# Kernel optimization log

Measured on AMD Instinct MI355X. Metric: run time of the kernel, lower is better.

## Reference

```python
import jax, jax.numpy as jnp
import numpy as np

B, NCAMS = 1, 6
C_FEAT = 64                     # fusion_feat_in_dim
H, W = 88, 160                  # per-camera feature map size at fusion level
VOX_SIZE = (100, 100, 20)       # (x_dim, y_dim, z_dim) voxel counts
VOX_STR = (-50.0, -50.0, -15.0)
VOX_UNIT = (1.0, 1.0, 1.5)
N_VOX = VOX_SIZE[0] * VOX_SIZE[1] * VOX_SIZE[2]
EPS = 1e-8
V_PRE = 64                      # voxel_pre_dim[0]


def make_voxel_pts(dtype):
    # [B, 4, N]; homogeneous (x, y, z, 1) points, layout [z, y, x] flattened
    xs = jnp.linspace(VOX_STR[0], VOX_STR[0] + VOX_UNIT[0] * (VOX_SIZE[0] - 1), VOX_SIZE[0], dtype=dtype)
    ys = jnp.linspace(VOX_STR[1], VOX_STR[1] + VOX_UNIT[1] * (VOX_SIZE[1] - 1), VOX_SIZE[1], dtype=dtype)
    zs = jnp.linspace(VOX_STR[2], VOX_STR[2] + VOX_UNIT[2] * (VOX_SIZE[2] - 1), VOX_SIZE[2], dtype=dtype)
    zdim, ydim, xdim = VOX_SIZE[2], VOX_SIZE[1], VOX_SIZE[0]
    gx = jnp.broadcast_to(xs[None, None, :], (zdim, ydim, xdim)).reshape(-1)
    gy = jnp.broadcast_to(ys[None, :, None], (zdim, ydim, xdim)).reshape(-1)
    gz = jnp.broadcast_to(zs[:, None, None], (zdim, ydim, xdim)).reshape(-1)
    pts = jnp.stack([gx, gy, gz, jnp.ones_like(gx)], axis=0)  # [4, N]
    return jnp.broadcast_to(pts[None], (B, 4, N_VOX))


def _gather(imgf, iy, ix, Wd):
    # imgf: [BN, C, H*W]; iy/ix: [BN, N] int32 -> [BN, C, N]
    lin = iy * Wd + ix
    return jnp.take_along_axis(imgf, lin[:, None, :], axis=2)


def bilinear_sample(img, gx, gy):
    # grid_sample(mode='bilinear', padding_mode='zeros', align_corners=True)
    BN, C, Hd, Wd = img.shape
    x = (gx + 1.0) * 0.5 * (Wd - 1)
    y = (gy + 1.0) * 0.5 * (Hd - 1)
    x0 = jnp.floor(x); y0 = jnp.floor(y)
    wx1 = x - x0; wx0 = 1.0 - wx1
    wy1 = y - y0; wy0 = 1.0 - wy1
    imgf = img.reshape(BN, C, Hd * Wd)
    out = jnp.zeros((BN, C, gx.shape[1]), dtype=img.dtype)
    for xi, wxi in ((x0, wx0), (x0 + 1.0, wx1)):
        for yi, wyi in ((y0, wy0), (y0 + 1.0, wy1)):
            valid = (xi >= 0) & (xi <= Wd - 1) & (yi >= 0) & (yi <= Hd - 1)
            ii = jnp.clip(xi, 0, Wd - 1).astype(jnp.int32)
            jj = jnp.clip(yi, 0, Hd - 1).astype(jnp.int32)
            w = (wxi * wyi * valid.astype(img.dtype))[:, None, :]
            out = out + _gather(imgf, jj, ii, Wd) * w
    return out


def nearest_sample(img, gx, gy):
    # grid_sample(mode='nearest', padding_mode='zeros', align_corners=True)
    BN, C, Hd, Wd = img.shape
    x = (gx + 1.0) * 0.5 * (Wd - 1)
    y = (gy + 1.0) * 0.5 * (Hd - 1)
    xi = jnp.round(x); yi = jnp.round(y)
    valid = (xi >= 0) & (xi <= Wd - 1) & (yi >= 0) & (yi <= Hd - 1)
    ii = jnp.clip(xi, 0, Wd - 1).astype(jnp.int32)
    jj = jnp.clip(yi, 0, Hd - 1).astype(jnp.int32)
    imgf = img.reshape(BN, C, Hd * Wd)
    return _gather(imgf, jj, ii, Wd) * valid[:, None, :].astype(img.dtype)


def setup_inputs() -> dict:
    key = jax.random.key(0)
    ks = jax.random.split(key, 8)
    return {
        'multi_img_feat': jax.random.normal(ks[0], (B, NCAMS, C_FEAT, H, W), jnp.float32),
        'mask': jax.random.uniform(ks[1], (B, NCAMS, 1, H, W), jnp.float32),
        'K': jax.random.normal(ks[2], (B, NCAMS, 4, 4), jnp.float32),
        'extrinsics': jax.random.normal(ks[3], (B, NCAMS, 4, 4), jnp.float32),
        'w_no': jax.random.normal(ks[4], (V_PRE, C_FEAT + 1), jnp.float32) * 0.05,
        'b_no': jax.random.normal(ks[5], (V_PRE,), jnp.float32) * 0.05,
        'w_o': jax.random.normal(ks[6], (V_PRE, 2 * (C_FEAT + 1)), jnp.float32) * 0.05,
        'b_o': jax.random.normal(ks[7], (V_PRE,), jnp.float32) * 0.05,
    }


def reference(multi_img_feat, mask, K, extrinsics, w_no, b_no, w_o, b_o):
    Bb, NC, C, Hd, Wd = multi_img_feat.shape
    dt = multi_img_feat.dtype
    vpts = make_voxel_pts(dt)                                          # [B,4,N]
    vpts_c = jnp.broadcast_to(vpts[:, None], (Bb, NC, 4, N_VOX)).reshape(Bb * NC, 4, N_VOX)
    feats = multi_img_feat.reshape(Bb * NC, C, Hd, Wd)
    masks = mask.reshape(Bb * NC, 1, Hd, Wd)                           # interp to (H,W) is identity (same size, align_corners)
    ext = extrinsics.reshape(Bb * NC, 4, 4)[:, :3, :]
    K3 = K.reshape(Bb * NC, 4, 4)[:, :3, :3]

    v_local = jnp.einsum('bij,bjn->bin', ext, vpts_c)                  # [BN,3,N]
    cam_pts = jnp.einsum('bij,bjn->bin', K3, v_local)
    pix = cam_pts[:, :2] / (cam_pts[:, 2:3] + EPS)
    pix = jnp.where(jnp.all(jnp.isfinite(pix)), pix, jnp.clip(pix, -Wd * 2.0, Wd * 2.0))
    gx = (pix[:, 0] / (Wd - 1) - 0.5) * 2.0                            # [BN,N] normalized coords
    gy = (pix[:, 1] / (Hd - 1) - 0.5) * 2.0

    feat_w = bilinear_sample(feats, gx, gy)                            # [BN,C,N]
    m_occ = nearest_sample(masks, gx, gy) > 0.5                        # [BN,1,N]
    m_depth = v_local[:, 2:3] > 0
    oob = (gx > 1) | (gx < -1) | (gy > 1) | (gy < -1)
    valid = (m_occ & m_depth & (~oob)[:, None, :]).astype(dt)          # [BN,1,N]

    feat_w = jnp.concatenate([feat_w, v_local[:, 2:3] / VOX_SIZE[0]], axis=1) * valid  # [BN,C+1,N]

    feat_w = feat_w.reshape(Bb, NC, C + 1, N_VOX)
    valid = valid.reshape(Bb, NC, 1, N_VOX)
    count = valid.sum(axis=1)                                          # [B,1,N]

    # non-overlap branch: voxels seen by exactly one camera
    no_mask = (count == 1).astype(dt)
    vox_no = feat_w.sum(axis=1) * no_mask
    vox_no = jax.nn.elu(jnp.einsum('oc,bcn->bon', w_no, vox_no) + b_no[None, :, None]) * no_mask

    # overlap branch: cams {0,3,4} vs {1,2,5}
    o_mask = (count == 2).astype(dt)
    feat1 = feat_w[:, 0] + feat_w[:, 3] + feat_w[:, 4]
    feat2 = feat_w[:, 1] + feat_w[:, 2] + feat_w[:, 5]
    vox_o = jnp.concatenate([feat1, feat2], axis=1)                    # [B,2*(C+1),N]
    vox_o = jax.nn.elu(jnp.einsum('oc,bcn->bon', w_o, vox_o) + b_o[None, :, None]) * o_mask

    return vox_no + vox_o                                              # [B, V_PRE, N]
```

## Files before the change

### kernel.cpp

```cpp
#include <hip/hip_runtime.h>
#include <cmath>

#define NC 6
#define CF 64
#define HH 88
#define WW 160
#define NPIX 14080
#define NVOX 200000
#define VPRE 64
#define VB 128
#define NTH 512
#define NWV 8

typedef unsigned int u32;

#define FEATT_BYTES  (6u * 64u * 14080u * 4u)

__global__ __launch_bounds__(256) void transpose_feats(const float* __restrict__ in,
                                                       float* __restrict__ out) {
    __shared__ float tile[64 * 65];
    int blk = blockIdx.x;
    int c = blk / 220;
    int p0 = (blk - c * 220) * 64;
    int tid = threadIdx.x;
    int lane = tid & 63;
    int quad = tid >> 6;
    for (int r = quad; r < 64; r += 4)
        tile[r * 65 + lane] = in[(c * 64 + r) * NPIX + p0 + lane];
    __syncthreads();
    for (int r = quad; r < 64; r += 4)
        out[((c * NPIX) + p0 + r) * 64 + lane] = tile[lane * 65 + r];
}

__device__ __forceinline__ float elu1(float x) { return x > 0.0f ? x : expm1f(x); }

__device__ __forceinline__ float gather_bilin(const float* __restrict__ fsrc, int useT,
                                              int lane, int cam, float x, float y) {
    float x0f = floorf(x), y0f = floorf(y);
    float wx1 = x - x0f, wx0 = 1.0f - wx1;
    float wy1 = y - y0f, wy0 = 1.0f - wy1;
    float x1f = x0f + 1.0f, y1f = y0f + 1.0f;
    float bx0 = (x0f >= 0.0f && x0f <= 159.0f) ? 1.0f : 0.0f;
    float bx1 = (x1f >= 0.0f && x1f <= 159.0f) ? 1.0f : 0.0f;
    float by0 = (y0f >= 0.0f && y0f <= 87.0f) ? 1.0f : 0.0f;
    float by1 = (y1f >= 0.0f && y1f <= 87.0f) ? 1.0f : 0.0f;
    int ix0 = (int)fminf(fmaxf(x0f, 0.0f), 159.0f);
    int ix1 = (int)fminf(fmaxf(x1f, 0.0f), 159.0f);
    int iy0 = (int)fminf(fmaxf(y0f, 0.0f), 87.0f);
    int iy1 = (int)fminf(fmaxf(y1f, 0.0f), 87.0f);
    int A = useT ? 64 : 1;
    int Boff = useT ? (cam * NPIX * 64 + lane) : ((cam * 64 + lane) * NPIX);
    float v00 = fsrc[(iy0 * WW + ix0) * A + Boff];
    float v01 = fsrc[(iy1 * WW + ix0) * A + Boff];
    float v10 = fsrc[(iy0 * WW + ix1) * A + Boff];
    float v11 = fsrc[(iy1 * WW + ix1) * A + Boff];
    float fv;
    fv  = (wx0 * wy0 * bx0 * by0) * v00;
    fv += (wx0 * wy1 * bx0 * by1) * v01;
    fv += (wx1 * wy0 * bx1 * by0) * v10;
    fv += (wx1 * wy1 * bx1 * by1) * v11;
    return fv;
}

#define FMA8_STEP(W0,W1,W2,W3,W4,W5,W6,W7,CG,F0,F1,F2,F3) \
    a0 += W0[CG]*F0; a0 += W0[CG+1]*F1; a0 += W0[CG+2]*F2; a0 += W0[CG+3]*F3; \
    a1 += W1[CG]*F0; a1 += W1[CG+1]*F1; a1 += W1[CG+2]*F2; a1 += W1[CG+3]*F3; \
    a2 += W2[CG]*F0; a2 += W2[CG+1]*F1; a2 += W2[CG+2]*F2; a2 += W2[CG+3]*F3; \
    a3 += W3[CG]*F0; a3 += W3[CG+1]*F1; a3 += W3[CG+2]*F2; a3 += W3[CG+3]*F3; \
    a4 += W4[CG]*F0; a4 += W4[CG+1]*F1; a4 += W4[CG+2]*F2; a4 += W4[CG+3]*F3; \
    a5 += W5[CG]*F0; a5 += W5[CG+1]*F1; a5 += W5[CG+2]*F2; a5 += W5[CG+3]*F3; \
    a6 += W6[CG]*F0; a6 += W6[CG+1]*F1; a6 += W6[CG+2]*F2; a6 += W6[CG+3]*F3; \
    a7 += W7[CG]*F0; a7 += W7[CG+1]*F1; a7 += W7[CG+2]*F2; a7 += W7[CG+3]*F3;

#define STORE8(COL) \
    outp[(size_t)(obase + 0) * NVOX + COL] = elu1(a0); \
    outp[(size_t)(obase + 1) * NVOX + COL] = elu1(a1); \
    outp[(size_t)(obase + 2) * NVOX + COL] = elu1(a2); \
    outp[(size_t)(obase + 3) * NVOX + COL] = elu1(a3); \
    outp[(size_t)(obase + 4) * NVOX + COL] = elu1(a4); \
    outp[(size_t)(obase + 5) * NVOX + COL] = elu1(a5); \
    outp[(size_t)(obase + 6) * NVOX + COL] = elu1(a6); \
    outp[(size_t)(obase + 7) * NVOX + COL] = elu1(a7);

__global__ __launch_bounds__(NTH) void vox_fused(
    const float* __restrict__ feats,
    const float* __restrict__ featT,
    const float* __restrict__ mask,
    const float* __restrict__ Kg,
    const float* __restrict__ ext,
    const float* __restrict__ wno,
    const float* __restrict__ bno,
    const float* __restrict__ wo,
    const float* __restrict__ bo,
    float* __restrict__ outp,
    int useT)
{
    __shared__ float s_ext[72];
    __shared__ float s_K[54];
    __shared__ float s_F[65 * 66];
    __shared__ __align__(16) float4 s_rec1[VB];
    __shared__ __align__(16) float4 s_rec2[2 * VB];
    __shared__ int s_vox[64];
    __shared__ int s_n1, s_n2;

    int tid = threadIdx.x;
    int lane = tid & 63;
    int wv = tid >> 6;
    int base = blockIdx.x * VB;
    int vlim = min(VB, NVOX - base);

    if (tid == 0) { s_n1 = 0; s_n2 = 0; }
    if (tid >= 64 && tid < 136) {
        int i = tid - 64;
        s_ext[i] = ext[(i / 12) * 16 + (i % 12)];
    }
    if (tid >= 192 && tid < 246) {
        int i = tid - 192; int cam = i / 9; int e = i - cam * 9;
        s_K[i] = Kg[cam * 16 + (e / 3) * 4 + (e % 3)];
    }

    {
        int ng4 = vlim >> 2;
        for (int i = tid; i < 64 * (VB / 4); i += NTH) {
            int r = i >> 5, cg = i & ((VB / 4) - 1);
            if (cg < ng4)
                *(float4*)(outp + (size_t)r * NVOX + base + (cg << 2)) =
                    make_float4(0.f, 0.f, 0.f, 0.f);
        }
    }
    __syncthreads();

    if (tid < vlim) {
        #pragma clang fp contract(off)
        int n = base + tid;
        int xi = n % 100;
        int t = n / 100;
        int yi = t % 100;
        int zi = t / 100;
        float X = -50.0f + (float)xi;
        float Y = -50.0f + (float)yi;
        float Z = -15.0f + 1.5f * (float)zi;
        int cnt = 0, cam0 = 0, cam1 = 0;
        float ax = 0.f, ay = 0.f, az = 0.f, bx = 0.f, by = 0.f, bz = 0.f;
        #pragma unroll
        for (int cam = 0; cam < NC; ++cam) {
            const float* E = s_ext + cam * 12;
            const float* Kk = s_K + cam * 9;
            float vl0 = E[0]*X + E[1]*Y + E[2]*Z + E[3];
            float vl1 = E[4]*X + E[5]*Y + E[6]*Z + E[7];
            float vl2 = E[8]*X + E[9]*Y + E[10]*Z + E[11];
            float c0 = Kk[0]*vl0 + Kk[1]*vl1 + Kk[2]*vl2;
            float c1 = Kk[3]*vl0 + Kk[4]*vl1 + Kk[5]*vl2;
            float c2 = Kk[6]*vl0 + Kk[7]*vl1 + Kk[8]*vl2;
            float pz = c2 + 1e-8f;
            float px = c0 / pz;
            float py = c1 / pz;
            float gx = (px / 159.0f - 0.5f) * 2.0f;
            float gy = (py / 87.0f - 0.5f) * 2.0f;
            float x = ((gx + 1.0f) * 0.5f) * 159.0f;
            float y = ((gy + 1.0f) * 0.5f) * 87.0f;
            float xr = rintf(x), yr = rintf(y);
            bool nv = (xr >= 0.0f) && (xr <= 159.0f) && (yr >= 0.0f) && (yr <= 87.0f);
            float mval = 0.0f;
            if (nv) mval = mask[(cam * HH + (int)yr) * WW + (int)xr];
            bool ok = (mval > 0.5f) && (vl2 > 0.0f) &&
                      !((gx > 1.0f) || (gx < -1.0f) || (gy > 1.0f) || (gy < -1.0f));
            if (ok) {
                if (cnt == 0) { ax = x; ay = y; az = vl2; cam0 = cam; }
                else if (cnt == 1) { bx = x; by = y; bz = vl2; cam1 = cam; }
                ++cnt;
            }
        }
        if (cnt == 1) {
            int s = atomicAdd(&s_n1, 1);
            s_rec1[s] = make_float4(ax, ay, az, __int_as_float((n << 3) | cam0));
        } else if (cnt == 2) {
            int s = atomicAdd(&s_n2, 1);
            s_rec2[2 * s + 0] = make_float4(ax, ay, az, __int_as_float((n << 3) | cam0));
            s_rec2[2 * s + 1] = make_float4(bx, by, bz, __int_as_float((n << 3) | cam1));
        }
    }
    __syncthreads();

    int n1 = s_n1, n2 = s_n2;
    const float* fsrc = useT ? featT : feats;
    int wvu = __builtin_amdgcn_readfirstlane(wv);
    int obase = wvu * 8;
    const float* w0n = wno + (obase + 0) * 65;
    const float* w1n = wno + (obase + 1) * 65;
    const float* w2n = wno + (obase + 2) * 65;
    const float* w3n = wno + (obase + 3) * 65;
    const float* w4n = wno + (obase + 4) * 65;
    const float* w5n = wno + (obase + 5) * 65;
    const float* w6n = wno + (obase + 6) * 65;
    const float* w7n = wno + (obase + 7) * 65;
    const float* w0o = wo + (obase + 0) * 130;
    const float* w1o = wo + (obase + 1) * 130;
    const float* w2o = wo + (obase + 2) * 130;
    const float* w3o = wo + (obase + 3) * 130;
    const float* w4o = wo + (obase + 4) * 130;
    const float* w5o = wo + (obase + 5) * 130;
    const float* w6o = wo + (obase + 6) * 130;
    const float* w7o = wo + (obase + 7) * 130;

    for (int t0 = 0; t0 < n1; t0 += 64) {
        int tl = min(64, n1 - t0);
        for (int e = wv; e < tl; e += NWV) {
            float4 r = s_rec1[t0 + e];
            int meta = __float_as_int(r.w);
            int cam = meta & 7;
            float fv = gather_bilin(fsrc, useT, lane, cam, r.x, r.y);
            s_F[lane * 66 + e] = fv;
            if (lane == 0) { s_F[64 * 66 + e] = r.z / 100.0f; s_vox[e] = meta >> 3; }
        }
        __syncthreads();
        float a0 = bno[obase + 0], a1 = bno[obase + 1], a2 = bno[obase + 2], a3 = bno[obase + 3];
        float a4 = bno[obase + 4], a5 = bno[obase + 5], a6 = bno[obase + 6], a7 = bno[obase + 7];
        for (int cg = 0; cg < 64; cg += 4) {
            float f0 = s_F[(cg + 0) * 66 + lane];
            float f1 = s_F[(cg + 1) * 66 + lane];
            float f2 = s_F[(cg + 2) * 66 + lane];
            float f3 = s_F[(cg + 3) * 66 + lane];
            FMA8_STEP(w0n, w1n, w2n, w3n, w4n, w5n, w6n, w7n, cg, f0, f1, f2, f3)
        }
        float fd = s_F[64 * 66 + lane];
        a0 += w0n[64] * fd; a1 += w1n[64] * fd; a2 += w2n[64] * fd; a3 += w3n[64] * fd;
        a4 += w4n[64] * fd; a5 += w5n[64] * fd; a6 += w6n[64] * fd; a7 += w7n[64] * fd;
        if (lane < tl) {
            size_t col = (size_t)s_vox[lane];
            STORE8(col)
        }
        __syncthreads();
    }

    for (int t0 = 0; t0 < n2; t0 += 64) {
        int tl = min(64, n2 - t0);
        for (int e = wv; e < tl; e += NWV) {
            float4 r0 = s_rec2[2 * (t0 + e) + 0];
            float4 r1 = s_rec2[2 * (t0 + e) + 1];
            int m0 = __float_as_int(r0.w), m1 = __float_as_int(r1.w);
            int ca = m0 & 7, cb = m1 & 7;
            float fg = 0.0f, dd = 0.0f;
            if (!(ca == 1 || ca == 2 || ca == 5)) {
                fg += gather_bilin(fsrc, useT, lane, ca, r0.x, r0.y);
                dd += r0.z / 100.0f;
            }
            if (!(cb == 1 || cb == 2 || cb == 5)) {
                fg += gather_bilin(fsrc, useT, lane, cb, r1.x, r1.y);
                dd += r1.z / 100.0f;
            }
            s_F[lane * 66 + e] = fg;
            if (lane == 0) { s_F[64 * 66 + e] = dd; s_vox[e] = m0 >> 3; }
        }
        __syncthreads();
        float a0 = bo[obase + 0], a1 = bo[obase + 1], a2 = bo[obase + 2], a3 = bo[obase + 3];
        float a4 = bo[obase + 4], a5 = bo[obase + 5], a6 = bo[obase + 6], a7 = bo[obase + 7];
        for (int cg = 0; cg < 64; cg += 4) {
            float f0 = s_F[(cg + 0) * 66 + lane];
            float f1 = s_F[(cg + 1) * 66 + lane];
            float f2 = s_F[(cg + 2) * 66 + lane];
            float f3 = s_F[(cg + 3) * 66 + lane];
            FMA8_STEP(w0o, w1o, w2o, w3o, w4o, w5o, w6o, w7o, cg, f0, f1, f2, f3)
        }
        {
            float fd = s_F[64 * 66 + lane];
            a0 += w0o[64] * fd; a1 += w1o[64] * fd; a2 += w2o[64] * fd; a3 += w3o[64] * fd;
            a4 += w4o[64] * fd; a5 += w5o[64] * fd; a6 += w6o[64] * fd; a7 += w7o[64] * fd;
        }
        __syncthreads();
        for (int e = wv; e < tl; e += NWV) {
            float4 r0 = s_rec2[2 * (t0 + e) + 0];
            float4 r1 = s_rec2[2 * (t0 + e) + 1];
            int m0 = __float_as_int(r0.w), m1 = __float_as_int(r1.w);
            int ca = m0 & 7, cb = m1 & 7;
            float fg = 0.0f, dd = 0.0f;
            if (ca == 1 || ca == 2 || ca == 5) {
                fg += gather_bilin(fsrc, useT, lane, ca, r0.x, r0.y);
                dd += r0.z / 100.0f;
            }
            if (cb == 1 || cb == 2 || cb == 5) {
                fg += gather_bilin(fsrc, useT, lane, cb, r1.x, r1.y);
                dd += r1.z / 100.0f;
            }
            s_F[lane * 66 + e] = fg;
            if (lane == 0) s_F[64 * 66 + e] = dd;
        }
        __syncthreads();
        for (int cg = 0; cg < 64; cg += 4) {
            float f0 = s_F[(cg + 0) * 66 + lane];
            float f1 = s_F[(cg + 1) * 66 + lane];
            float f2 = s_F[(cg + 2) * 66 + lane];
            float f3 = s_F[(cg + 3) * 66 + lane];
            int cgo = cg + 65;
            FMA8_STEP(w0o, w1o, w2o, w3o, w4o, w5o, w6o, w7o, cgo, f0, f1, f2, f3)
        }
        {
            float fd = s_F[64 * 66 + lane];
            a0 += w0o[129] * fd; a1 += w1o[129] * fd; a2 += w2o[129] * fd; a3 += w3o[129] * fd;
            a4 += w4o[129] * fd; a5 += w5o[129] * fd; a6 += w6o[129] * fd; a7 += w7o[129] * fd;
        }
        if (lane < tl) {
            size_t col = (size_t)s_vox[lane];
            STORE8(col)
        }
        __syncthreads();
    }
}

extern "C" void kernel_launch(void* const* d_in, const int* in_sizes, int n_in,
                              void* d_out, int out_size, void* d_ws, size_t ws_size,
                              hipStream_t stream) {
    const float* feats = (const float*)d_in[0];
    const float* mask  = (const float*)d_in[1];
    const float* Kg    = (const float*)d_in[2];
    const float* ext   = (const float*)d_in[3];
    const float* wno   = (const float*)d_in[4];
    const float* bno   = (const float*)d_in[5];
    const float* wo    = (const float*)d_in[6];
    const float* bo    = (const float*)d_in[7];
    float* outp = (float*)d_out;
    float* featT = (float*)d_ws;

    int useT = (ws_size >= (size_t)FEATT_BYTES) ? 1 : 0;
    if (useT) {
        transpose_feats<<<NC * 220, 256, 0, stream>>>(feats, featT);
    }
    int nblk = (NVOX + VB - 1) / VB;
    vox_fused<<<nblk, NTH, 0, stream>>>(feats, featT, mask, Kg, ext,
                                        wno, bno, wo, bo, outp, useT);
}
```

Before: 162.5 us.

## Defer overlap-voxel work to a compacted global queue processed by a second kernel

```diff
diff --git a/kernel.cpp b/kernel.cpp
--- a/kernel.cpp
+++ b/kernel.cpp
@@ -8,16 +8,21 @@
 #define NPIX 14080
 #define NVOX 200000
 #define VPRE 64
-#define VB 128
+#define VB 192
 #define NTH 512
 #define NWV 8
 
 typedef unsigned int u32;
 
 #define FEATT_BYTES  (6u * 64u * 14080u * 4u)
+#define REC2_OFF     FEATT_BYTES
+#define REC2_BYTES   (200000u * 32u)
+#define CNT_OFF      (REC2_OFF + REC2_BYTES)
+#define WS_NEED      (CNT_OFF + 16u)
 
 __global__ __launch_bounds__(256) void transpose_feats(const float* __restrict__ in,
-                                                       float* __restrict__ out) {
+                                                       float* __restrict__ out,
+                                                       int* __restrict__ cnt) {
     __shared__ float tile[64 * 65];
     int blk = blockIdx.x;
     int c = blk / 220;
@@ -25,6 +30,7 @@
     int tid = threadIdx.x;
     int lane = tid & 63;
     int quad = tid >> 6;
+    if (cnt && blk == 0 && tid == 0) cnt[0] = 0;
     for (int r = quad; r < 64; r += 4)
         tile[r * 65 + lane] = in[(c * 64 + r) * NPIX + p0 + lane];
     __syncthreads();
@@ -82,6 +88,26 @@
     outp[(size_t)(obase + 6) * NVOX + COL] = elu1(a6); \
     outp[(size_t)(obase + 7) * NVOX + COL] = elu1(a7);
 
+#define WNO_PTRS \
+    const float* w0n = wno + (obase + 0) * 65; \
+    const float* w1n = wno + (obase + 1) * 65; \
+    const float* w2n = wno + (obase + 2) * 65; \
+    const float* w3n = wno + (obase + 3) * 65; \
+    const float* w4n = wno + (obase + 4) * 65; \
+    const float* w5n = wno + (obase + 5) * 65; \
+    const float* w6n = wno + (obase + 6) * 65; \
+    const float* w7n = wno + (obase + 7) * 65;
+
+#define WO_PTRS \
+    const float* w0o = wo + (obase + 0) * 130; \
+    const float* w1o = wo + (obase + 1) * 130; \
+    const float* w2o = wo + (obase + 2) * 130; \
+    const float* w3o = wo + (obase + 3) * 130; \
+    const float* w4o = wo + (obase + 4) * 130; \
+    const float* w5o = wo + (obase + 5) * 130; \
+    const float* w6o = wo + (obase + 6) * 130; \
+    const float* w7o = wo + (obase + 7) * 130;
+
 __global__ __launch_bounds__(NTH) void vox_fused(
     const float* __restrict__ feats,
     const float* __restrict__ featT,
@@ -93,7 +119,9 @@
     const float* __restrict__ wo,
     const float* __restrict__ bo,
     float* __restrict__ outp,
-    int useT)
+    float4* __restrict__ grec2,
+    int* __restrict__ gcnt,
+    int useT, int defer2)
 {
     __shared__ float s_ext[72];
     __shared__ float s_K[54];
@@ -101,7 +129,7 @@
     __shared__ __align__(16) float4 s_rec1[VB];
     __shared__ __align__(16) float4 s_rec2[2 * VB];
     __shared__ int s_vox[64];
-    __shared__ int s_n1, s_n2;
+    __shared__ int s_n1, s_n2, s_base2;
 
     int tid = threadIdx.x;
     int lane = tid & 63;
@@ -110,19 +138,19 @@
     int vlim = min(VB, NVOX - base);
 
     if (tid == 0) { s_n1 = 0; s_n2 = 0; }
-    if (tid >= 64 && tid < 136) {
-        int i = tid - 64;
+    if (tid >= 256 && tid < 328) {
+        int i = tid - 256;
         s_ext[i] = ext[(i / 12) * 16 + (i % 12)];
     }
-    if (tid >= 192 && tid < 246) {
-        int i = tid - 192; int cam = i / 9; int e = i - cam * 9;
+    if (tid >= 384 && tid < 438) {
+        int i = tid - 384; int cam = i / 9; int e = i - cam * 9;
         s_K[i] = Kg[cam * 16 + (e / 3) * 4 + (e % 3)];
     }
 
     {
         int ng4 = vlim >> 2;
         for (int i = tid; i < 64 * (VB / 4); i += NTH) {
-            int r = i >> 5, cg = i & ((VB / 4) - 1);
+            int r = i / (VB / 4), cg = i - r * (VB / 4);
             if (cg < ng4)
                 *(float4*)(outp + (size_t)r * NVOX + base + (cg << 2)) =
                     make_float4(0.f, 0.f, 0.f, 0.f);
@@ -186,22 +214,17 @@
     const float* fsrc = useT ? featT : feats;
     int wvu = __builtin_amdgcn_readfirstlane(wv);
     int obase = wvu * 8;
-    const float* w0n = wno + (obase + 0) * 65;
-    const float* w1n = wno + (obase + 1) * 65;
-    const float* w2n = wno + (obase + 2) * 65;
-    const float* w3n = wno + (obase + 3) * 65;
-    const float* w4n = wno + (obase + 4) * 65;
-    const float* w5n = wno + (obase + 5) * 65;
-    const float* w6n = wno + (obase + 6) * 65;
-    const float* w7n = wno + (obase + 7) * 65;
-    const float* w0o = wo + (obase + 0) * 130;
-    const float* w1o = wo + (obase + 1) * 130;
-    const float* w2o = wo + (obase + 2) * 130;
-    const float* w3o = wo + (obase + 3) * 130;
-    const float* w4o = wo + (obase + 4) * 130;
-    const float* w5o = wo + (obase + 5) * 130;
-    const float* w6o = wo + (obase + 6) * 130;
-    const float* w7o = wo + (obase + 7) * 130;
+    WNO_PTRS
+
+    if (defer2) {
+        if (n2 > 0) {
+            if (tid == 0) s_base2 = atomicAdd(gcnt, n2);
+            __syncthreads();
+            int b2 = s_base2;
+            for (int i = tid; i < 2 * n2; i += NTH)
+                grec2[2 * b2 + i] = s_rec2[i];
+        }
+    }
 
     for (int t0 = 0; t0 < n1; t0 += 64) {
         int tl = min(64, n1 - t0);
@@ -233,11 +256,113 @@
         __syncthreads();
     }
 
-    for (int t0 = 0; t0 < n2; t0 += 64) {
-        int tl = min(64, n2 - t0);
+    if (!defer2) {
+        WO_PTRS
+        for (int t0 = 0; t0 < n2; t0 += 64) {
+            int tl = min(64, n2 - t0);
+            for (int e = wv; e < tl; e += NWV) {
+                float4 r0 = s_rec2[2 * (t0 + e) + 0];
+                float4 r1 = s_rec2[2 * (t0 + e) + 1];
+                int m0 = __float_as_int(r0.w), m1 = __float_as_int(r1.w);
+                int ca = m0 & 7, cb = m1 & 7;
+                float fg = 0.0f, dd = 0.0f;
+                if (!(ca == 1 || ca == 2 || ca == 5)) {
+                    fg += gather_bilin(fsrc, useT, lane, ca, r0.x, r0.y);
+                    dd += r0.z / 100.0f;
+                }
+                if (!(cb == 1 || cb == 2 || cb == 5)) {
+                    fg += gather_bilin(fsrc, useT, lane, cb, r1.x, r1.y);
+                    dd += r1.z / 100.0f;
+                }
+                s_F[lane * 66 + e] = fg;
+                if (lane == 0) { s_F[64 * 66 + e] = dd; s_vox[e] = m0 >> 3; }
+            }
+            __syncthreads();
+            float a0 = bo[obase + 0], a1 = bo[obase + 1], a2 = bo[obase + 2], a3 = bo[obase + 3];
+            float a4 = bo[obase + 4], a5 = bo[obase + 5], a6 = bo[obase + 6], a7 = bo[obase + 7];
+            for (int cg = 0; cg < 64; cg += 4) {
+                float f0 = s_F[(cg + 0) * 66 + lane];
+                float f1 = s_F[(cg + 1) * 66 + lane];
+                float f2 = s_F[(cg + 2) * 66 + lane];
+                float f3 = s_F[(cg + 3) * 66 + lane];
+                FMA8_STEP(w0o, w1o, w2o, w3o, w4o, w5o, w6o, w7o, cg, f0, f1, f2, f3)
+            }
+            {
+                float fd = s_F[64 * 66 + lane];
+                a0 += w0o[64] * fd; a1 += w1o[64] * fd; a2 += w2o[64] * fd; a3 += w3o[64] * fd;
+                a4 += w4o[64] * fd; a5 += w5o[64] * fd; a6 += w6o[64] * fd; a7 += w7o[64] * fd;
+            }
+            __syncthreads();
+            for (int e = wv; e < tl; e += NWV) {
+                float4 r0 = s_rec2[2 * (t0 + e) + 0];
+                float4 r1 = s_rec2[2 * (t0 + e) + 1];
+                int m0 = __float_as_int(r0.w), m1 = __float_as_int(r1.w);
+                int ca = m0 & 7, cb = m1 & 7;
+                float fg = 0.0f, dd = 0.0f;
+                if (ca == 1 || ca == 2 || ca == 5) {
+                    fg += gather_bilin(fsrc, useT, lane, ca, r0.x, r0.y);
+                    dd += r0.z / 100.0f;
+                }
+                if (cb == 1 || cb == 2 || cb == 5) {
+                    fg += gather_bilin(fsrc, useT, lane, cb, r1.x, r1.y);
+                    dd += r1.z / 100.0f;
+                }
+                s_F[lane * 66 + e] = fg;
+                if (lane == 0) s_F[64 * 66 + e] = dd;
+            }
+            __syncthreads();
+            for (int cg = 0; cg < 64; cg += 4) {
+                float f0 = s_F[(cg + 0) * 66 + lane];
+                float f1 = s_F[(cg + 1) * 66 + lane];
+                float f2 = s_F[(cg + 2) * 66 + lane];
+                float f3 = s_F[(cg + 3) * 66 + lane];
+                int cgo = cg + 65;
+                FMA8_STEP(w0o, w1o, w2o, w3o, w4o, w5o, w6o, w7o, cgo, f0, f1, f2, f3)
+            }
+            {
+                float fd = s_F[64 * 66 + lane];
+                a0 += w0o[129] * fd; a1 += w1o[129] * fd; a2 += w2o[129] * fd; a3 += w3o[129] * fd;
+                a4 += w4o[129] * fd; a5 += w5o[129] * fd; a6 += w6o[129] * fd; a7 += w7o[129] * fd;
+            }
+            if (lane < tl) {
+                size_t col = (size_t)s_vox[lane];
+                STORE8(col)
+            }
+            __syncthreads();
+        }
+    }
+}
+
+__global__ __launch_bounds__(NTH) void vox_ov(
+    const float* __restrict__ feats,
+    const float* __restrict__ featT,
+    const float4* __restrict__ rec2,
+    const int* __restrict__ gcnt,
+    const float* __restrict__ wo,
+    const float* __restrict__ bo,
+    float* __restrict__ outp,
+    int useT)
+{
+    __shared__ float s_F[65 * 66];
+    __shared__ int s_vox[64];
+
+    int tid = threadIdx.x;
+    int lane = tid & 63;
+    int wv = tid >> 6;
+    int c2 = gcnt[0];
+    int nt = (c2 + 63) >> 6;
+
+    const float* fsrc = useT ? featT : feats;
+    int wvu = __builtin_amdgcn_readfirstlane(wv);
+    int obase = wvu * 8;
+    WO_PTRS
+
+    for (int t = blockIdx.x; t < nt; t += gridDim.x) {
+        int e0 = t << 6;
+        int tl = min(64, c2 - e0);
         for (int e = wv; e < tl; e += NWV) {
-            float4 r0 = s_rec2[2 * (t0 + e) + 0];
-            float4 r1 = s_rec2[2 * (t0 + e) + 1];
+            float4 r0 = rec2[2 * (e0 + e) + 0];
+            float4 r1 = rec2[2 * (e0 + e) + 1];
             int m0 = __float_as_int(r0.w), m1 = __float_as_int(r1.w);
             int ca = m0 & 7, cb = m1 & 7;
             float fg = 0.0f, dd = 0.0f;
@@ -269,8 +394,8 @@
         }
         __syncthreads();
         for (int e = wv; e < tl; e += NWV) {
-            float4 r0 = s_rec2[2 * (t0 + e) + 0];
-            float4 r1 = s_rec2[2 * (t0 + e) + 1];
+            float4 r0 = rec2[2 * (e0 + e) + 0];
+            float4 r1 = rec2[2 * (e0 + e) + 1];
             int m0 = __float_as_int(r0.w), m1 = __float_as_int(r1.w);
             int ca = m0 & 7, cb = m1 & 7;
             float fg = 0.0f, dd = 0.0f;
@@ -319,13 +444,23 @@
     const float* wo    = (const float*)d_in[6];
     const float* bo    = (const float*)d_in[7];
     float* outp = (float*)d_out;
-    float* featT = (float*)d_ws;
+    char* wsb = (char*)d_ws;
+    float* featT = (float*)wsb;
 
     int useT = (ws_size >= (size_t)FEATT_BYTES) ? 1 : 0;
+    int defer2 = (ws_size >= (size_t)WS_NEED) ? 1 : 0;
+    float4* grec2 = defer2 ? (float4*)(wsb + REC2_OFF) : nullptr;
+    int* gcnt = defer2 ? (int*)(wsb + CNT_OFF) : nullptr;
+
     if (useT) {
-        transpose_feats<<<NC * 220, 256, 0, stream>>>(feats, featT);
+        transpose_feats<<<NC * 220, 256, 0, stream>>>(feats, featT, gcnt);
     }
     int nblk = (NVOX + VB - 1) / VB;
     vox_fused<<<nblk, NTH, 0, stream>>>(feats, featT, mask, Kg, ext,
-                                        wno, bno, wo, bo, outp, useT);
+                                        wno, bno, wo, bo, outp,
+                                        grec2, gcnt, useT, defer2);
+    if (defer2) {
+        vox_ov<<<256, NTH, 0, stream>>>(feats, featT, grec2, gcnt,
+                                        wo, bo, outp, useT);
+    }
 }
```

Result: slower. 174.4 us (+7.3%).

## Unroll bilinear gather loops, batch LDS feature reads, and enlarge voxel block

Applied to the files above, without the earlier changes.

```diff
diff --git a/kernel.cpp b/kernel.cpp
--- a/kernel.cpp
+++ b/kernel.cpp
@@ -8,7 +8,7 @@
 #define NPIX 14080
 #define NVOX 200000
 #define VPRE 64
-#define VB 128
+#define VB 192
 #define NTH 512
 #define NWV 8
 
@@ -82,6 +82,18 @@
     outp[(size_t)(obase + 6) * NVOX + COL] = elu1(a6); \
     outp[(size_t)(obase + 7) * NVOX + COL] = elu1(a7);
 
+#define COMPUTE_HALF(WB0,WB1,WB2,WB3,WB4,WB5,WB6,WB7,CBASE) \
+    { \
+        float f[32]; \
+        _Pragma("unroll") \
+        for (int c = 0; c < 32; ++c) f[c] = s_F[(CBASE + c) * 66 + lane]; \
+        _Pragma("unroll") \
+        for (int cg = 0; cg < 32; cg += 4) { \
+            FMA8_STEP(WB0,WB1,WB2,WB3,WB4,WB5,WB6,WB7, (CBASE + cg), \
+                      f[cg], f[cg+1], f[cg+2], f[cg+3]) \
+        } \
+    }
+
 __global__ __launch_bounds__(NTH) void vox_fused(
     const float* __restrict__ feats,
     const float* __restrict__ featT,
@@ -110,19 +122,19 @@
     int vlim = min(VB, NVOX - base);
 
     if (tid == 0) { s_n1 = 0; s_n2 = 0; }
-    if (tid >= 64 && tid < 136) {
-        int i = tid - 64;
+    if (tid >= 256 && tid < 328) {
+        int i = tid - 256;
         s_ext[i] = ext[(i / 12) * 16 + (i % 12)];
     }
-    if (tid >= 192 && tid < 246) {
-        int i = tid - 192; int cam = i / 9; int e = i - cam * 9;
+    if (tid >= 384 && tid < 438) {
+        int i = tid - 384; int cam = i / 9; int e = i - cam * 9;
         s_K[i] = Kg[cam * 16 + (e / 3) * 4 + (e % 3)];
     }
 
     {
         int ng4 = vlim >> 2;
         for (int i = tid; i < 64 * (VB / 4); i += NTH) {
-            int r = i >> 5, cg = i & ((VB / 4) - 1);
+            int r = i / (VB / 4), cg = i - r * (VB / 4);
             if (cg < ng4)
                 *(float4*)(outp + (size_t)r * NVOX + base + (cg << 2)) =
                     make_float4(0.f, 0.f, 0.f, 0.f);
@@ -205,24 +217,25 @@
 
     for (int t0 = 0; t0 < n1; t0 += 64) {
         int tl = min(64, n1 - t0);
-        for (int e = wv; e < tl; e += NWV) {
-            float4 r = s_rec1[t0 + e];
+        int tl1 = tl - 1;
+        #pragma unroll
+        for (int j = 0; j < 8; ++j) {
+            int e = wv + j * NWV;
+            int ee = min(e, tl1);
+            float4 r = s_rec1[t0 + ee];
             int meta = __float_as_int(r.w);
             int cam = meta & 7;
             float fv = gather_bilin(fsrc, useT, lane, cam, r.x, r.y);
-            s_F[lane * 66 + e] = fv;
-            if (lane == 0) { s_F[64 * 66 + e] = r.z / 100.0f; s_vox[e] = meta >> 3; }
+            if (e < tl) {
+                s_F[lane * 66 + e] = fv;
+                if (lane == 0) { s_F[64 * 66 + e] = r.z / 100.0f; s_vox[e] = meta >> 3; }
+            }
         }
         __syncthreads();
         float a0 = bno[obase + 0], a1 = bno[obase + 1], a2 = bno[obase + 2], a3 = bno[obase + 3];
         float a4 = bno[obase + 4], a5 = bno[obase + 5], a6 = bno[obase + 6], a7 = bno[obase + 7];
-        for (int cg = 0; cg < 64; cg += 4) {
-            float f0 = s_F[(cg + 0) * 66 + lane];
-            float f1 = s_F[(cg + 1) * 66 + lane];
-            float f2 = s_F[(cg + 2) * 66 + lane];
-            float f3 = s_F[(cg + 3) * 66 + lane];
-            FMA8_STEP(w0n, w1n, w2n, w3n, w4n, w5n, w6n, w7n, cg, f0, f1, f2, f3)
-        }
+        COMPUTE_HALF(w0n, w1n, w2n, w3n, w4n, w5n, w6n, w7n, 0)
+        COMPUTE_HALF(w0n, w1n, w2n, w3n, w4n, w5n, w6n, w7n, 32)
         float fd = s_F[64 * 66 + lane];
         a0 += w0n[64] * fd; a1 += w1n[64] * fd; a2 += w2n[64] * fd; a3 += w3n[64] * fd;
         a4 += w4n[64] * fd; a5 += w5n[64] * fd; a6 += w6n[64] * fd; a7 += w7n[64] * fd;
@@ -235,9 +248,13 @@
 
     for (int t0 = 0; t0 < n2; t0 += 64) {
         int tl = min(64, n2 - t0);
-        for (int e = wv; e < tl; e += NWV) {
-            float4 r0 = s_rec2[2 * (t0 + e) + 0];
-            float4 r1 = s_rec2[2 * (t0 + e) + 1];
+        int tl1 = tl - 1;
+        #pragma unroll
+        for (int j = 0; j < 8; ++j) {
+            int e = wv + j * NWV;
+            int ee = min(e, tl1);
+            float4 r0 = s_rec2[2 * (t0 + ee) + 0];
+            float4 r1 = s_rec2[2 * (t0 + ee) + 1];
             int m0 = __float_as_int(r0.w), m1 = __float_as_int(r1.w);
             int ca = m0 & 7, cb = m1 & 7;
             float fg = 0.0f, dd = 0.0f;
@@ -249,28 +266,28 @@
                 fg += gather_bilin(fsrc, useT, lane, cb, r1.x, r1.y);
                 dd += r1.z / 100.0f;
             }
-            s_F[lane * 66 + e] = fg;
-            if (lane == 0) { s_F[64 * 66 + e] = dd; s_vox[e] = m0 >> 3; }
+            if (e < tl) {
+                s_F[lane * 66 + e] = fg;
+                if (lane == 0) { s_F[64 * 66 + e] = dd; s_vox[e] = m0 >> 3; }
+            }
         }
         __syncthreads();
         float a0 = bo[obase + 0], a1 = bo[obase + 1], a2 = bo[obase + 2], a3 = bo[obase + 3];
         float a4 = bo[obase + 4], a5 = bo[obase + 5], a6 = bo[obase + 6], a7 = bo[obase + 7];
-        for (int cg = 0; cg < 64; cg += 4) {
-            float f0 = s_F[(cg + 0) * 66 + lane];
-            float f1 = s_F[(cg + 1) * 66 + lane];
-            float f2 = s_F[(cg + 2) * 66 + lane];
-            float f3 = s_F[(cg + 3) * 66 + lane];
-            FMA8_STEP(w0o, w1o, w2o, w3o, w4o, w5o, w6o, w7o, cg, f0, f1, f2, f3)
-        }
+        COMPUTE_HALF(w0o, w1o, w2o, w3o, w4o, w5o, w6o, w7o, 0)
+        COMPUTE_HALF(w0o, w1o, w2o, w3o, w4o, w5o, w6o, w7o, 32)
         {
             float fd = s_F[64 * 66 + lane];
             a0 += w0o[64] * fd; a1 += w1o[64] * fd; a2 += w2o[64] * fd; a3 += w3o[64] * fd;
             a4 += w4o[64] * fd; a5 += w5o[64] * fd; a6 += w6o[64] * fd; a7 += w7o[64] * fd;
         }
         __syncthreads();
-        for (int e = wv; e < tl; e += NWV) {
-            float4 r0 = s_rec2[2 * (t0 + e) + 0];
-            float4 r1 = s_rec2[2 * (t0 + e) + 1];
+        #pragma unroll
+        for (int j = 0; j < 8; ++j) {
+            int e = wv + j * NWV;
+            int ee = min(e, tl1);
+            float4 r0 = s_rec2[2 * (t0 + ee) + 0];
+            float4 r1 = s_rec2[2 * (t0 + ee) + 1];
             int m0 = __float_as_int(r0.w), m1 = __float_as_int(r1.w);
             int ca = m0 & 7, cb = m1 & 7;
             float fg = 0.0f, dd = 0.0f;
@@ -282,17 +299,28 @@
                 fg += gather_bilin(fsrc, useT, lane, cb, r1.x, r1.y);
                 dd += r1.z / 100.0f;
             }
-            s_F[lane * 66 + e] = fg;
-            if (lane == 0) s_F[64 * 66 + e] = dd;
-        }
-        __syncthreads();
-        for (int cg = 0; cg < 64; cg += 4) {
-            float f0 = s_F[(cg + 0) * 66 + lane];
-            float f1 = s_F[(cg + 1) * 66 + lane];
-            float f2 = s_F[(cg + 2) * 66 + lane];
-            float f3 = s_F[(cg + 3) * 66 + lane];
-            int cgo = cg + 65;
-            FMA8_STEP(w0o, w1o, w2o, w3o, w4o, w5o, w6o, w7o, cgo, f0, f1, f2, f3)
+            if (e < tl) {
+                s_F[lane * 66 + e] = fg;
+                if (lane == 0) s_F[64 * 66 + e] = dd;
+            }
+        }
+        __syncthreads();
+        {
+            float f[32];
+            #pragma unroll
+            for (int c = 0; c < 32; ++c) f[c] = s_F[c * 66 + lane];
+            #pragma unroll
+            for (int cg = 0; cg < 32; cg += 4) {
+                FMA8_STEP(w0o, w1o, w2o, w3o, w4o, w5o, w6o, w7o, (65 + cg),
+                          f[cg], f[cg+1], f[cg+2], f[cg+3])
+            }
+            #pragma unroll
+            for (int c = 0; c < 32; ++c) f[c] = s_F[(32 + c) * 66 + lane];
+            #pragma unroll
+            for (int cg = 0; cg < 32; cg += 4) {
+                FMA8_STEP(w0o, w1o, w2o, w3o, w4o, w5o, w6o, w7o, (97 + cg),
+                          f[cg], f[cg+1], f[cg+2], f[cg+3])
+            }
         }
         {
             float fd = s_F[64 * 66 + lane];
```

New measurement: 249.5 us. 1.54x slower.
